# Kernel optimization log

Measured on AMD Instinct MI355X. Metric: run time of the kernel, lower is better.

The kernel has to match this reference:

```python
import jax, jax.numpy as jnp
import numpy as np

B, T, C, HS = 8, 4096, 512, 64

def setup_inputs() -> dict:
    key = jax.random.key(0)
    k1, k2, k3, k4 = jax.random.split(key, 4)
    x = jax.random.normal(k1, (B, T, C), dtype=jnp.float32)
    # causal mask (lower-triangular), int32: 1 = keep, 0 = mask out
    mask = jnp.tril(jnp.ones((T, T), dtype=jnp.int32))
    Wk = jax.random.normal(k2, (C, HS), dtype=jnp.float32) * (1.0 / np.sqrt(C))
    Wq = jax.random.normal(k3, (C, HS), dtype=jnp.float32) * (1.0 / np.sqrt(C))
    Wv = jax.random.normal(k4, (C, HS), dtype=jnp.float32) * (1.0 / np.sqrt(C))
    return {"x": x, "mask": mask, "Wk": Wk, "Wq": Wq, "Wv": Wv}

def reference(x, mask, Wk, Wq, Wv):
    # single self-attention head; scale uses C (n_embd), matching the source
    k = jnp.einsum('btc,ch->bth', x, Wk)   # [B,T,HS]
    q = jnp.einsum('btc,ch->bth', x, Wq)
    v = jnp.einsum('btc,ch->bth', x, Wv)
    scale = x.shape[-1] ** -0.5
    wei = jnp.einsum('bth,bsh->bts', q, k) * scale          # [B,T,T]
    wei = jnp.where(mask == 0, jnp.float32(-1e9), wei)
    wei = jax.nn.softmax(wei, axis=-1)
    # dropout is identity in eval mode
    out = jnp.einsum('bts,bsh->bth', wei, v)                # [B,T,HS]
    return out
```

## Files before the change

### kernel.cpp

```cpp
#include <hip/hip_runtime.h>
#include <hip/hip_bf16.h>
#include <stdint.h>

typedef unsigned short u16;
typedef __bf16 bf16x8_t __attribute__((ext_vector_type(8)));
typedef __bf16 bf16x4_t __attribute__((ext_vector_type(4)));
typedef float f32x4_t __attribute__((ext_vector_type(4)));
typedef float f32x8_t __attribute__((ext_vector_type(8)));
typedef float f32x16_t __attribute__((ext_vector_type(16)));
typedef int i32x2_t __attribute__((ext_vector_type(2)));

#define TSEQ 4096
#define CDIM 512
#define HSD  64
#define NBATCH 8

static __device__ __forceinline__ f32x4_t mfma16(bf16x8_t a, bf16x8_t b, f32x4_t c) {
  return __builtin_amdgcn_mfma_f32_16x16x32_bf16(a, b, c, 0, 0, 0);
}
static __device__ __forceinline__ f32x16_t mfma32(bf16x8_t a, bf16x8_t b, f32x16_t c) {
  return __builtin_amdgcn_mfma_f32_32x32x16_bf16(a, b, c, 0, 0, 0);
}

static __device__ __forceinline__ u16 f2bf(float f) {
  union { __bf16 h; u16 s; } v; v.h = (__bf16)f;
  return v.s;
}
static __device__ __forceinline__ float bf2f(u16 h) {
  union { unsigned u; float f; } v; v.u = ((unsigned)h) << 16;
  return v.f;
}
static __device__ __forceinline__ bf16x4_t cvt4(f32x4_t v) {
  return __builtin_convertvector(v, bf16x4_t);
}

static __device__ __forceinline__ void gload16(const void* g, void* l) {
  __builtin_amdgcn_global_load_lds(
      (const __attribute__((address_space(1))) unsigned int*)g,
      (__attribute__((address_space(3))) unsigned int*)l, 16, 0, 0);
}

#define QSCALE (0.044194173824159216f * 1.4426950408889634f)
#define MFIX 32.0f

__global__ __launch_bounds__(256) void repack_w(const float* __restrict__ Wk,
                                                const float* __restrict__ Wq,
                                                const float* __restrict__ Wv,
                                                u16* __restrict__ pw) {
  int i = blockIdx.x * 256 + threadIdx.x;
  int j    = i & 7;
  int l15  = (i >> 3) & 15;
  int quad = (i >> 7) & 3;
  int f    = i >> 9;
  int kc   = f / 12;
  int n12  = f - kc * 12;
  int m    = n12 >> 2;
  int n    = n12 & 3;
  const float* W = (m == 0) ? Wk : ((m == 1) ? Wq : Wv);
  pw[i] = f2bf(W[(kc * 32 + quad * 8 + j) * HSD + n * 16 + l15]);
}

__global__ __launch_bounds__(256, 2) void proj_kernel(const float* __restrict__ x,
                                                      const u16* __restrict__ pw,
                                                      u16* __restrict__ kb,
                                                      u16* __restrict__ qb,
                                                      u16* __restrict__ vb,
                                                      u16* __restrict__ vbT,
                                                      int split) {
  const int tid = threadIdx.x;
  const int lane = tid & 63;
  const int wave = tid >> 6;
  const int l15 = lane & 15, quad = lane >> 4;
  const int rblk = (int)blockIdx.x;
  const int rowLocal = wave * 16 + l15;

  __shared__ __align__(16) char SMEM[61440];
  float (*XS)[2048] = (float (*)[2048])SMEM;
  u16   (*PS)[6144] = (u16 (*)[6144])(SMEM + 24576);
  u16* VtS = (u16*)SMEM;

  const float* xg = x + (size_t)rblk * 64 * CDIM;

  const int xrow = tid >> 3;
  const int xch  = tid & 7;

  f32x4_t acc[12];
#pragma unroll
  for (int n = 0; n < 12; ++n) acc[n] = f32x4_t{0.f, 0.f, 0.f, 0.f};

  auto STAGE = [&](int slot, int kc) {
#pragma unroll
    for (int p = 0; p < 2; ++p) {
      const float* src = xg + (size_t)(p * 32 + xrow) * CDIM + kc * 32 + xch * 4;
      gload16(src, (char*)&XS[slot][0] + p * 4096 + tid * 16);
    }
#pragma unroll
    for (int r = 0; r < 3; ++r) {
      int f = r * 256 + tid;
      gload16(pw + (size_t)kc * 6144 + (size_t)f * 8, (char*)&PS[slot][0] + f * 16);
    }
  };

  STAGE(0, 0);
  STAGE(1, 1);

  int slot = 0;
  for (int kc = 0; kc < 16; ++kc) {
    if (kc < 15) asm volatile("s_waitcnt vmcnt(5)" ::: "memory");
    else         asm volatile("s_waitcnt vmcnt(0)" ::: "memory");
    __builtin_amdgcn_s_barrier();

    if (kc + 2 < 16) {
      int s2 = slot + 2; if (s2 >= 3) s2 -= 3;
      STAGE(s2, kc + 2);
    }

    f32x8_t xv = *(const f32x8_t*)&XS[slot][rowLocal * 32 + quad * 8];
    bf16x8_t a = __builtin_convertvector(xv, bf16x8_t);
#pragma unroll
    for (int n12 = 0; n12 < 12; ++n12) {
      bf16x8_t b = *(const bf16x8_t*)&PS[slot][((n12 * 4 + quad) * 16 + l15) * 8];
      acc[n12] = mfma16(a, b, acc[n12]);
    }

    ++slot; if (slot >= 3) slot = 0;
  }

  const int row_base = rblk * 64 + wave * 16 + quad * 4;
#pragma unroll
  for (int n = 0; n < 4; ++n) {
#pragma unroll
    for (int r = 0; r < 4; ++r) {
      kb[(size_t)(row_base + r) * HSD + n * 16 + l15] = f2bf(acc[n][r]);
      qb[(size_t)(row_base + r) * HSD + n * 16 + l15] = f2bf(acc[4 + n][r] * QSCALE);
    }
  }

  if (!split) {
#pragma unroll
    for (int n = 0; n < 4; ++n)
#pragma unroll
      for (int r = 0; r < 4; ++r)
        vb[(size_t)(row_base + r) * HSD + n * 16 + l15] = f2bf(acc[8 + n][r]);
  } else {
    __syncthreads();
#pragma unroll
    for (int n = 0; n < 4; ++n) {
      int h = n * 16 + l15;
      int tl = wave * 16 + quad * 4;
      *(bf16x4_t*)&VtS[h * 72 + tl] = cvt4(acc[8 + n]);
    }
    __syncthreads();
    const int bb = (rblk * 64) >> 12;
    const int t0 = (rblk * 64) & 4095;
#pragma unroll
    for (int it = 0; it < 2; ++it) {
      int g = it * 256 + tid;
      int h = g >> 3;
      int cc = g & 7;
      bf16x8_t vv = *(const bf16x8_t*)&VtS[h * 72 + cc * 8];
      *(bf16x8_t*)&vbT[(size_t)(bb * HSD + h) * TSEQ + t0 + cc * 8] = vv;
    }
  }
}

__global__ __launch_bounds__(256, 4) void attn_part(const u16* __restrict__ qb,
                                                    const u16* __restrict__ kb,
                                                    const u16* __restrict__ vbT,
                                                    u16* __restrict__ pO,
                                                    float* __restrict__ pl) {
  const int e = 143 - (int)blockIdx.x;
  int g = 0;
  while (g < 7 && 2 * (g + 1) * (g + 2) <= e) ++g;
  int local = e - 2 * g * (g + 1);
  int qtl = 0;
  while (local >= g + 1) { local -= g + 1; ++qtl; }
  const int qt2 = 4 * g + qtl;
  const int c   = local;

  const int b = blockIdx.y;
  const int tid = threadIdx.x;
  const int lane = tid & 63;
  const int wave = tid >> 6;
  const int l31 = lane & 31;
  const int h2  = lane >> 5;

  __shared__ __align__(16) char LDS[32768];

  const size_t bo = (size_t)b * TSEQ * HSD;
  const u16* qp = qb + bo;
  const u16* kp = kb + bo;
  const u16* vtp = vbT + (size_t)b * HSD * TSEQ;

  const int qglob = qt2 * 128 + wave * 32 + l31;
  const int wdiag = (qt2 * 128 + wave * 32 + 31) >> 6;

  bf16x8_t qf[4];
#pragma unroll
  for (int kk = 0; kk < 4; ++kk)
    qf[kk] = *(const bf16x8_t*)(qp + (size_t)qglob * HSD + kk * 16 + h2 * 8);

  f32x16_t o0, o1;
#pragma unroll
  for (int i = 0; i < 16; ++i) { o0[i] = 0.f; o1[i] = 0.f; }
  float lsum = 0.f;

  const int st_lo = c * 8;
  const int nt = min(2 * qt2 + 2 - st_lo, 8);

  const int c0 = l31 & 7;
  int A[4];
#pragma unroll
  for (int j = 0; j < 4; ++j) A[j] = l31 * 128 + (((j * 2 + h2) ^ c0) << 4);

  const u16* ksrc[2];
  const u16* vsrc[2];
#pragma unroll
  for (int i = 0; i < 2; ++i) {
    int q = wave * 128 + i * 64 + lane;
    int row = q >> 3, cl = (q & 7) ^ (row & 7);
    ksrc[i] = kp + (size_t)(st_lo * 64 + row) * HSD + cl * 8;
    vsrc[i] = vtp + (size_t)row * TSEQ + st_lo * 64 + cl * 8;
  }

  auto DMA = [&](int t) {
    const int buf = t & 1;
    char* kd = LDS + buf * 8192 + wave * 2048;
    char* vd = LDS + 16384 + buf * 8192 + wave * 2048;
    gload16(ksrc[0] + (size_t)t * 64 * HSD, kd);
    gload16(ksrc[1] + (size_t)t * 64 * HSD, kd + 1024);
    gload16(vsrc[0] + (size_t)t * 64, vd);
    gload16(vsrc[1] + (size_t)t * 64, vd + 1024);
  };

  DMA(0);
  DMA(1);

  auto TILE = [&](int t, int buf) {
    if (t + 1 < nt) asm volatile("s_waitcnt vmcnt(4)" ::: "memory");
    else            asm volatile("s_waitcnt vmcnt(0)" ::: "memory");
    __builtin_amdgcn_s_barrier();

    const int stx = st_lo + t;
    if (stx <= wdiag) {
      const char* kbase = LDS + buf * 8192;
      const char* vbase = LDS + 16384 + buf * 8192;
#pragma unroll
      for (int st2 = 0; st2 < 2; ++st2) {
        f32x16_t s;
#pragma unroll
        for (int i = 0; i < 16; ++i) s[i] = -MFIX;
#pragma unroll
        for (int kk = 0; kk < 4; ++kk) {
          bf16x8_t a = *(const bf16x8_t*)(kbase + st2 * 4096 + A[kk]);
          s = mfma32(a, qf[kk], s);
        }

        if (stx == wdiag) {
#pragma unroll
          for (int i = 0; i < 16; ++i) {
            int sg = stx * 64 + st2 * 32 + 4 * h2 + (i & 3) + 8 * (i >> 2);
            if (sg > qglob) s[i] = -1e9f;
          }
        }

#pragma unroll
        for (int i = 0; i < 16; ++i) s[i] = exp2f(s[i]);
#pragma unroll
        for (int i = 0; i < 16; i += 4)
          lsum += ((s[i] + s[i + 1]) + (s[i + 2] + s[i + 3]));

        union { bf16x4_t v; int d[2]; } X[4];
#pragma unroll
        for (int m = 0; m < 4; ++m) {
          f32x4_t tt;
          tt[0] = s[4 * m]; tt[1] = s[4 * m + 1]; tt[2] = s[4 * m + 2]; tt[3] = s[4 * m + 3];
          X[m].v = cvt4(tt);
        }

#pragma unroll
        for (int kkl = 0; kkl < 2; ++kkl) {
          i32x2_t r0 = __builtin_amdgcn_permlane32_swap(X[2 * kkl].d[0], X[2 * kkl + 1].d[0], false, false);
          i32x2_t r1 = __builtin_amdgcn_permlane32_swap(X[2 * kkl].d[1], X[2 * kkl + 1].d[1], false, false);
          union { bf16x8_t v; int d[4]; } af;
          af.d[0] = r0[0]; af.d[1] = r1[0];
          af.d[2] = r0[1]; af.d[3] = r1[1];
          const int kkg = st2 * 2 + kkl;
          bf16x8_t vf0 = *(const bf16x8_t*)(vbase + A[kkg]);
          bf16x8_t vf1 = *(const bf16x8_t*)(vbase + 4096 + A[kkg]);
          o0 = mfma32(af.v, vf0, o0);
          o1 = mfma32(af.v, vf1, o1);
        }
      }
    }

    __builtin_amdgcn_s_barrier();
    if (t + 2 < nt) DMA(t + 2);
  };

  for (int ip = 0; ip < (nt >> 1); ++ip) {
    TILE(2 * ip, 0);
    TILE(2 * ip + 1, 1);
  }

  lsum += __shfl_xor(lsum, 32);

  const int pidx = (b * 64 + 2 * qt2 + (wave >> 1)) * 8 + c;
  u16* po = pO + (size_t)pidx * 4096;
  float* pm = pl + (size_t)pidx * 64;
#pragma unroll
  for (int i = 0; i < 16; ++i) {
    int rloc = (wave & 1) * 32 + 4 * h2 + (i & 3) + 8 * (i >> 2);
    po[rloc * 64 + l31]      = f2bf(o0[i]);
    po[rloc * 64 + 32 + l31] = f2bf(o1[i]);
  }
  if (lane < 32) pm[(wave & 1) * 32 + lane] = lsum;
}

__global__ __launch_bounds__(256) void attn_combine(const u16* __restrict__ pO,
                                                    const float* __restrict__ pl,
                                                    float* __restrict__ out) {
  const int tid = threadIdx.x;
  const int h2 = tid & 31;
  const int rr = tid >> 5;
  const int rowg = blockIdx.x * 8 + rr;
  const int b = rowg >> 12;
  const int t = rowg & 4095;
  const int qt = t >> 6;
  const int tr = t & 63;
  const int nc = (qt >> 3) + 1;
  const int pbase = (b * 64 + qt) * 8;

  const unsigned* pO32 = (const unsigned*)pO;
  float o0 = 0.f, o1 = 0.f, lsum = 0.f;
  for (int cc = 0; cc < nc; ++cc) {
    lsum += pl[(size_t)(pbase + cc) * 64 + tr];
    unsigned u = pO32[(size_t)(pbase + cc) * 2048 + tr * 32 + h2];
    o0 += bf2f((u16)(u & 0xffffu));
    o1 += bf2f((u16)(u >> 16));
  }
  float2 res;
  res.x = o0 / lsum;
  res.y = o1 / lsum;
  *(float2*)&out[(size_t)rowg * HSD + h2 * 2] = res;
}

__global__ __launch_bounds__(256) void attn_single(const u16* __restrict__ qb,
                                                   const u16* __restrict__ kb,
                                                   const u16* __restrict__ vb,
                                                   float* __restrict__ out) {
  const int qt = (int)gridDim.x - 1 - (int)blockIdx.x;
  const int b = blockIdx.y;
  const int lane = threadIdx.x & 63;
  const int wave = threadIdx.x >> 6;
  const int l15 = lane & 15, quad = lane >> 4;

  __shared__ __align__(16) u16 Ks[64 * 72];
  __shared__ __align__(16) u16 Vt[64 * 72];
  __shared__ __align__(16) u16 Ps[4][16 * 72];

  const size_t bo = (size_t)b * TSEQ * HSD;
  const u16* qp = qb + bo;
  const u16* kp = kb + bo;
  const u16* vp = vb + bo;

  const int qrow0 = qt * 64 + wave * 16;
  bf16x8_t qf0 = *(const bf16x8_t*)(qp + (size_t)(qrow0 + l15) * HSD + quad * 8);
  bf16x8_t qf1 = *(const bf16x8_t*)(qp + (size_t)(qrow0 + l15) * HSD + 32 + quad * 8);

  f32x4_t o[4];
#pragma unroll
  for (int n = 0; n < 4; ++n) o[n] = f32x4_t{0.f, 0.f, 0.f, 0.f};
  float lrow[4] = {0.f, 0.f, 0.f, 0.f};

  const int ldr = threadIdx.x >> 3;
  const int ldc = (threadIdx.x & 7) * 8;

  const f32x4_t sinit = f32x4_t{-MFIX, -MFIX, -MFIX, -MFIX};

  for (int st = 0; st <= qt; ++st) {
    const int s0 = st * 64;
#pragma unroll
    for (int pp = 0; pp < 2; ++pp) {
      int r = ldr + pp * 32;
      bf16x8_t kv = *(const bf16x8_t*)(kp + (size_t)(s0 + r) * HSD + ldc);
      *(bf16x8_t*)&Ks[r * 72 + ldc] = kv;
      bf16x8_t vv = *(const bf16x8_t*)(vp + (size_t)(s0 + r) * HSD + ldc);
      const u16* vu = (const u16*)&vv;
#pragma unroll
      for (int j = 0; j < 8; ++j) Vt[(ldc + j) * 72 + r] = vu[j];
    }
    __syncthreads();

    f32x4_t s[4];
#pragma unroll
    for (int n = 0; n < 4; ++n) {
      bf16x8_t k0 = *(const bf16x8_t*)&Ks[(n * 16 + l15) * 72 + quad * 8];
      bf16x8_t k1 = *(const bf16x8_t*)&Ks[(n * 16 + l15) * 72 + 32 + quad * 8];
      f32x4_t a = sinit;
      a = mfma16(qf0, k0, a);
      a = mfma16(qf1, k1, a);
      s[n] = a;
    }

    if (st == qt) {
#pragma unroll
      for (int n = 0; n < 4; ++n) {
        int sg = s0 + n * 16 + l15;
#pragma unroll
        for (int r = 0; r < 4; ++r) {
          int tg = qrow0 + quad * 4 + r;
          if (sg > tg) s[n][r] = -1e9f;
        }
      }
    }

#pragma unroll
    for (int n = 0; n < 4; ++n)
#pragma unroll
      for (int r = 0; r < 4; ++r) {
        float p = exp2f(s[n][r]);
        s[n][r] = p;
        lrow[r] += p;
      }

    u16* myP = Ps[wave];
#pragma unroll
    for (int n = 0; n < 4; ++n)
#pragma unroll
      for (int r = 0; r < 4; ++r)
        myP[(quad * 4 + r) * 72 + n * 16 + l15] = f2bf(s[n][r]);

    __syncthreads();

#pragma unroll
    for (int kc = 0; kc < 2; ++kc) {
      bf16x8_t pf = *(const bf16x8_t*)&myP[l15 * 72 + kc * 32 + quad * 8];
#pragma unroll
      for (int n = 0; n < 4; ++n) {
        bf16x8_t vf = *(const bf16x8_t*)&Vt[(n * 16 + l15) * 72 + kc * 32 + quad * 8];
        o[n] = mfma16(pf, vf, o[n]);
      }
    }
    __syncthreads();
  }

#pragma unroll
  for (int r = 0; r < 4; ++r) {
    float l = lrow[r];
    l += __shfl_xor(l, 1);
    l += __shfl_xor(l, 2);
    l += __shfl_xor(l, 4);
    l += __shfl_xor(l, 8);
    lrow[r] = l;
  }

#pragma unroll
  for (int n = 0; n < 4; ++n)
#pragma unroll
    for (int r = 0; r < 4; ++r)
      out[bo + (size_t)(qrow0 + quad * 4 + r) * HSD + n * 16 + l15] = o[n][r] / lrow[r];
}

extern "C" void kernel_launch(void* const* d_in, const int* in_sizes, int n_in,
                              void* d_out, int out_size, void* d_ws, size_t ws_size,
                              hipStream_t stream) {
  const float* x  = (const float*)d_in[0];
  const float* Wk = (const float*)d_in[2];
  const float* Wq = (const float*)d_in[3];
  const float* Wv = (const float*)d_in[4];
  float* out = (float*)d_out;

  char* base = (char*)d_ws;
  const size_t KV = (size_t)NBATCH * TSEQ * HSD;
  u16* pw  = (u16*)base;
  u16* kb  = (u16*)(base + (1 << 18));
  u16* qb  = kb + KV;
  u16* vbT = qb + KV;
  u16* pO  = vbT + KV;
  u16* vb  = pO;
  float* pl = (float*)(pO + (size_t)4096 * 4096);
  const size_t need = (size_t)(1 << 18) + 3 * KV * 2
                    + (size_t)4096 * 4096 * 2
                    + (size_t)4096 * 64 * 4;
  const int split = (ws_size >= need) ? 1 : 0;

  hipLaunchKernelGGL(repack_w, dim3(384), dim3(256), 0, stream, Wk, Wq, Wv, pw);
  hipLaunchKernelGGL(proj_kernel, dim3(512), dim3(256), 0, stream, x, pw, kb, qb, vb, vbT, split);
  if (split) {
    hipLaunchKernelGGL(attn_part, dim3(144, NBATCH), dim3(256), 0, stream, qb, kb, vbT, pO, pl);
    hipLaunchKernelGGL(attn_combine, dim3(4096), dim3(256), 0, stream, pO, pl, out);
  } else {
    hipLaunchKernelGGL(attn_single, dim3(64, NBATCH), dim3(256), 0, stream, qb, kb, vb, out);
  }
}
```

Measured before the change: 191.5 us.

## Triple-buffer K/V tiles in LDS and drop trailing barrier per tile

Switches the K/V shared-memory staging from double to triple buffering (32KB to 48KB LDS). The prefetch for tile t+2 is now issued right after the start-of-tile barrier instead of after a second barrier at the end. This removes one workgroup barrier per tile and lets loads overlap more of the compute. In exchange the kernel uses more LDS, which may lower occupancy, and the loop is no longer manually unrolled by two.

```diff
diff --git a/kernel.cpp b/kernel.cpp
--- a/kernel.cpp
+++ b/kernel.cpp
@@ -185,7 +185,7 @@
   const int l31 = lane & 31;
   const int h2  = lane >> 5;
 
-  __shared__ __align__(16) char LDS[32768];
+  __shared__ __align__(16) char LDS[49152];
 
   const size_t bo = (size_t)b * TSEQ * HSD;
   const u16* qp = qb + bo;
@@ -223,28 +223,32 @@
     vsrc[i] = vtp + (size_t)row * TSEQ + st_lo * 64 + cl * 8;
   }
 
-  auto DMA = [&](int t) {
-    const int buf = t & 1;
-    char* kd = LDS + buf * 8192 + wave * 2048;
-    char* vd = LDS + 16384 + buf * 8192 + wave * 2048;
+  auto DMA = [&](int t, int bf) {
+    char* kd = LDS + bf * 16384 + wave * 2048;
     gload16(ksrc[0] + (size_t)t * 64 * HSD, kd);
     gload16(ksrc[1] + (size_t)t * 64 * HSD, kd + 1024);
-    gload16(vsrc[0] + (size_t)t * 64, vd);
-    gload16(vsrc[1] + (size_t)t * 64, vd + 1024);
+    gload16(vsrc[0] + (size_t)t * 64, kd + 8192);
+    gload16(vsrc[1] + (size_t)t * 64, kd + 8192 + 1024);
   };
 
-  DMA(0);
-  DMA(1);
-
-  auto TILE = [&](int t, int buf) {
+  DMA(0, 0);
+  DMA(1, 1);
+
+  int buf = 0;
+  for (int t = 0; t < nt; ++t) {
     if (t + 1 < nt) asm volatile("s_waitcnt vmcnt(4)" ::: "memory");
     else            asm volatile("s_waitcnt vmcnt(0)" ::: "memory");
     __builtin_amdgcn_s_barrier();
 
+    if (t + 2 < nt) {
+      int b2 = buf + 2; if (b2 >= 3) b2 -= 3;
+      DMA(t + 2, b2);
+    }
+
     const int stx = st_lo + t;
     if (stx <= wdiag) {
-      const char* kbase = LDS + buf * 8192;
-      const char* vbase = LDS + 16384 + buf * 8192;
+      const char* kbase = LDS + buf * 16384;
+      const char* vbase = kbase + 8192;
 #pragma unroll
       for (int st2 = 0; st2 < 2; ++st2) {
         f32x16_t s;
@@ -294,13 +298,7 @@
       }
     }
 
-    __builtin_amdgcn_s_barrier();
-    if (t + 2 < nt) DMA(t + 2);
-  };
-
-  for (int ip = 0; ip < (nt >> 1); ++ip) {
-    TILE(2 * ip, 0);
-    TILE(2 * ip + 1, 1);
+    ++buf; if (buf >= 3) buf = 0;
   }
 
   lsum += __shfl_xor(lsum, 32);
```

Measured after the change: 196.0 us. 1.02x slower.

## Fuse weight repack into projection and combine into attention via atomic counters

Applied to the files above, without the earlier changes.

Drops the separate weight-repack kernel: the projection kernel now reads fp32 weights directly from global memory with strided loads and converts them to bf16 in registers. Drops the separate combine kernel: single-chunk query tiles write normalized output directly, and for multi-chunk tiles the last-arriving block, found with an atomic counter, reduces the partials. This removes two kernel launches and the repack round trip. In exchange it adds uncoalesced per-lane weight loads inside the projection inner loop and a serialized tail reduction in one block per tile.

```diff
diff --git a/kernel.cpp b/kernel.cpp
--- a/kernel.cpp
+++ b/kernel.cpp
@@ -43,29 +43,15 @@
 #define QSCALE (0.044194173824159216f * 1.4426950408889634f)
 #define MFIX 32.0f
 
-__global__ __launch_bounds__(256) void repack_w(const float* __restrict__ Wk,
-                                                const float* __restrict__ Wq,
-                                                const float* __restrict__ Wv,
-                                                u16* __restrict__ pw) {
-  int i = blockIdx.x * 256 + threadIdx.x;
-  int j    = i & 7;
-  int l15  = (i >> 3) & 15;
-  int quad = (i >> 7) & 3;
-  int f    = i >> 9;
-  int kc   = f / 12;
-  int n12  = f - kc * 12;
-  int m    = n12 >> 2;
-  int n    = n12 & 3;
-  const float* W = (m == 0) ? Wk : ((m == 1) ? Wq : Wv);
-  pw[i] = f2bf(W[(kc * 32 + quad * 8 + j) * HSD + n * 16 + l15]);
-}
-
 __global__ __launch_bounds__(256, 2) void proj_kernel(const float* __restrict__ x,
-                                                      const u16* __restrict__ pw,
+                                                      const float* __restrict__ Wk,
+                                                      const float* __restrict__ Wq,
+                                                      const float* __restrict__ Wv,
                                                       u16* __restrict__ kb,
                                                       u16* __restrict__ qb,
                                                       u16* __restrict__ vb,
                                                       u16* __restrict__ vbT,
+                                                      unsigned* __restrict__ cnt,
                                                       int split) {
   const int tid = threadIdx.x;
   const int lane = tid & 63;
@@ -74,12 +60,14 @@
   const int rblk = (int)blockIdx.x;
   const int rowLocal = wave * 16 + l15;
 
-  __shared__ __align__(16) char SMEM[61440];
+  if (rblk < 256 && tid == 0) cnt[rblk] = 0;
+
+  __shared__ __align__(16) char SMEM[24576];
   float (*XS)[2048] = (float (*)[2048])SMEM;
-  u16   (*PS)[6144] = (u16 (*)[6144])(SMEM + 24576);
   u16* VtS = (u16*)SMEM;
 
   const float* xg = x + (size_t)rblk * 64 * CDIM;
+  const float* W3[3] = {Wk, Wq, Wv};
 
   const int xrow = tid >> 3;
   const int xch  = tid & 7;
@@ -94,11 +82,6 @@
       const float* src = xg + (size_t)(p * 32 + xrow) * CDIM + kc * 32 + xch * 4;
       gload16(src, (char*)&XS[slot][0] + p * 4096 + tid * 16);
     }
-#pragma unroll
-    for (int r = 0; r < 3; ++r) {
-      int f = r * 256 + tid;
-      gload16(pw + (size_t)kc * 6144 + (size_t)f * 8, (char*)&PS[slot][0] + f * 16);
-    }
   };
 
   STAGE(0, 0);
@@ -106,7 +89,7 @@
 
   int slot = 0;
   for (int kc = 0; kc < 16; ++kc) {
-    if (kc < 15) asm volatile("s_waitcnt vmcnt(5)" ::: "memory");
+    if (kc < 15) asm volatile("s_waitcnt vmcnt(2)" ::: "memory");
     else         asm volatile("s_waitcnt vmcnt(0)" ::: "memory");
     __builtin_amdgcn_s_barrier();
 
@@ -117,10 +100,16 @@
 
     f32x8_t xv = *(const f32x8_t*)&XS[slot][rowLocal * 32 + quad * 8];
     bf16x8_t a = __builtin_convertvector(xv, bf16x8_t);
+
 #pragma unroll
     for (int n12 = 0; n12 < 12; ++n12) {
-      bf16x8_t b = *(const bf16x8_t*)&PS[slot][((n12 * 4 + quad) * 16 + l15) * 8];
-      acc[n12] = mfma16(a, b, acc[n12]);
+      const float* wb = W3[n12 >> 2] + (size_t)(kc * 32 + quad * 8) * HSD
+                      + (n12 & 3) * 16 + l15;
+      f32x8_t wv;
+#pragma unroll
+      for (int j = 0; j < 8; ++j) wv[j] = wb[j * HSD];
+      bf16x8_t bfr = __builtin_convertvector(wv, bf16x8_t);
+      acc[n12] = mfma16(a, bfr, acc[n12]);
     }
 
     ++slot; if (slot >= 3) slot = 0;
@@ -168,7 +157,9 @@
                                                     const u16* __restrict__ kb,
                                                     const u16* __restrict__ vbT,
                                                     u16* __restrict__ pO,
-                                                    float* __restrict__ pl) {
+                                                    float* __restrict__ pl,
+                                                    unsigned* __restrict__ cnt,
+                                                    float* __restrict__ out) {
   const int e = 143 - (int)blockIdx.x;
   int g = 0;
   while (g < 7 && 2 * (g + 1) * (g + 2) <= e) ++g;
@@ -305,6 +296,20 @@
 
   lsum += __shfl_xor(lsum, 32);
 
+  const int nc2 = (qt2 >> 2) + 1;
+
+  if (nc2 == 1) {
+#pragma unroll
+    for (int i = 0; i < 16; ++i) {
+      int dl = 4 * h2 + (i & 3) + 8 * (i >> 2);
+      float inv = 1.0f / __shfl(lsum, dl);
+      size_t ro = ((size_t)b * TSEQ + qt2 * 128 + wave * 32 + dl) * HSD;
+      out[ro + l31]      = o0[i] * inv;
+      out[ro + 32 + l31] = o1[i] * inv;
+    }
+    return;
+  }
+
   const int pidx = (b * 64 + 2 * qt2 + (wave >> 1)) * 8 + c;
   u16* po = pO + (size_t)pidx * 4096;
   float* pm = pl + (size_t)pidx * 64;
@@ -315,34 +320,38 @@
     po[rloc * 64 + 32 + l31] = f2bf(o1[i]);
   }
   if (lane < 32) pm[(wave & 1) * 32 + lane] = lsum;
-}
-
-__global__ __launch_bounds__(256) void attn_combine(const u16* __restrict__ pO,
-                                                    const float* __restrict__ pl,
-                                                    float* __restrict__ out) {
-  const int tid = threadIdx.x;
-  const int h2 = tid & 31;
-  const int rr = tid >> 5;
-  const int rowg = blockIdx.x * 8 + rr;
-  const int b = rowg >> 12;
-  const int t = rowg & 4095;
-  const int qt = t >> 6;
-  const int tr = t & 63;
-  const int nc = (qt >> 3) + 1;
-  const int pbase = (b * 64 + qt) * 8;
-
-  const unsigned* pO32 = (const unsigned*)pO;
-  float o0 = 0.f, o1 = 0.f, lsum = 0.f;
-  for (int cc = 0; cc < nc; ++cc) {
-    lsum += pl[(size_t)(pbase + cc) * 64 + tr];
-    unsigned u = pO32[(size_t)(pbase + cc) * 2048 + tr * 32 + h2];
-    o0 += bf2f((u16)(u & 0xffffu));
-    o1 += bf2f((u16)(u >> 16));
-  }
-  float2 res;
-  res.x = o0 / lsum;
-  res.y = o1 / lsum;
-  *(float2*)&out[(size_t)rowg * HSD + h2 * 2] = res;
+
+  __threadfence();
+  unsigned* flagp = (unsigned*)LDS;
+  if (tid == 0) {
+    unsigned old = __hip_atomic_fetch_add(&cnt[b * 32 + qt2], 1u,
+                                          __ATOMIC_ACQ_REL,
+                                          __HIP_MEMORY_SCOPE_AGENT);
+    *flagp = (old == (unsigned)(nc2 - 1)) ? 1u : 0u;
+  }
+  __syncthreads();
+  if (*flagp) {
+    __threadfence();
+    const unsigned* pO32 = (const unsigned*)pO;
+    const int hh = tid & 31;
+    const int rr8 = tid >> 5;
+    for (int rowl = rr8; rowl < 128; rowl += 8) {
+      int qt = 2 * qt2 + (rowl >> 6);
+      int tr = rowl & 63;
+      int pb = (b * 64 + qt) * 8;
+      float a0 = 0.f, a1 = 0.f, ls = 0.f;
+      for (int cc = 0; cc < nc2; ++cc) {
+        ls += pl[(size_t)(pb + cc) * 64 + tr];
+        unsigned u = pO32[(size_t)(pb + cc) * 2048 + tr * 32 + hh];
+        a0 += bf2f((u16)(u & 0xffffu));
+        a1 += bf2f((u16)(u >> 16));
+      }
+      float2 res;
+      res.x = a0 / ls;
+      res.y = a1 / ls;
+      *(float2*)&out[((size_t)b * TSEQ + qt * 64 + tr) * HSD + hh * 2] = res;
+    }
+  }
 }
 
 __global__ __launch_bounds__(256) void attn_single(const u16* __restrict__ qb,
@@ -473,23 +482,24 @@
 
   char* base = (char*)d_ws;
   const size_t KV = (size_t)NBATCH * TSEQ * HSD;
-  u16* pw  = (u16*)base;
-  u16* kb  = (u16*)(base + (1 << 18));
+  u16* kb  = (u16*)base;
   u16* qb  = kb + KV;
   u16* vbT = qb + KV;
   u16* pO  = vbT + KV;
   u16* vb  = pO;
   float* pl = (float*)(pO + (size_t)4096 * 4096);
-  const size_t need = (size_t)(1 << 18) + 3 * KV * 2
+  unsigned* cnt = (unsigned*)(pl + (size_t)4096 * 64);
+  const size_t need = 3 * KV * 2
                     + (size_t)4096 * 4096 * 2
-                    + (size_t)4096 * 64 * 4;
+                    + (size_t)4096 * 64 * 4
+                    + 1024;
   const int split = (ws_size >= need) ? 1 : 0;
 
-  hipLaunchKernelGGL(repack_w, dim3(384), dim3(256), 0, stream, Wk, Wq, Wv, pw);
-  hipLaunchKernelGGL(proj_kernel, dim3(512), dim3(256), 0, stream, x, pw, kb, qb, vb, vbT, split);
+  hipLaunchKernelGGL(proj_kernel, dim3(512), dim3(256), 0, stream,
+                     x, Wk, Wq, Wv, kb, qb, vb, vbT, cnt, split);
   if (split) {
-    hipLaunchKernelGGL(attn_part, dim3(144, NBATCH), dim3(256), 0, stream, qb, kb, vbT, pO, pl);
-    hipLaunchKernelGGL(attn_combine, dim3(4096), dim3(256), 0, stream, pO, pl, out);
+    hipLaunchKernelGGL(attn_part, dim3(144, NBATCH), dim3(256), 0, stream,
+                       qb, kb, vbT, pO, pl, cnt, out);
   } else {
     hipLaunchKernelGGL(attn_single, dim3(64, NBATCH), dim3(256), 0, stream, qb, kb, vb, out);
   }
```

After: 473.7 us. 2.47x slower.
